# Optimization experiments

Measured on AMD Instinct MI355X. Metric: run time of the kernel, lower is better.

## Reference

```python
import jax, jax.numpy as jnp
import numpy as np

B, P, N = 64, 100, 1000
D, H, QD = 128, 8, 16
NUM_GROUPS = 5
MAX_DELTA = 4
SQRT_EMB = float(np.sqrt(D))
CLIP = 10.0
BIAS_INIT = 0.2
BIAS_TAU = 1.0


def setup_inputs() -> dict:
    key = jax.random.key(0)
    ks = jax.random.split(key, 12)
    w_scale = 1.0 / np.sqrt(D)
    encoded_nodes = jax.random.normal(ks[0], (B, N, D), dtype=jnp.float32)
    encoded_q1 = jax.random.normal(ks[1], (B, P, D), dtype=jnp.float32)
    encoded_last_node = jax.random.normal(ks[2], (B, P, D), dtype=jnp.float32)
    ninf_mask = jnp.where(jax.random.uniform(ks[3], (B, P, N)) < 0.2,
                          -jnp.inf, 0.0).astype(jnp.float32)
    Wq_first = (jax.random.normal(ks[4], (D, H * QD)) * w_scale).astype(jnp.float32)
    Wq_last = (jax.random.normal(ks[5], (D, H * QD)) * w_scale).astype(jnp.float32)
    Wk = (jax.random.normal(ks[6], (D, H * QD)) * w_scale).astype(jnp.float32)
    Wv = (jax.random.normal(ks[7], (D, H * QD)) * w_scale).astype(jnp.float32)
    W_comb = (jax.random.normal(ks[8], (H * QD, D)) * w_scale).astype(jnp.float32)
    b_comb = jnp.zeros((D,), dtype=jnp.float32)
    # learnable priority-bias table, init = 0.2 * exp(-delta / tau)
    deltas = jnp.arange(MAX_DELTA + 1, dtype=jnp.float32)
    bias_table = (BIAS_INIT * jnp.exp(-deltas / BIAS_TAU)).astype(jnp.float32)
    group_ids = jax.random.randint(ks[10], (B, N), 0, NUM_GROUPS).astype(jnp.int32)
    current_min_priority = jax.random.randint(ks[11], (B, P), 0, NUM_GROUPS).astype(jnp.int32)
    return {
        'encoded_nodes': encoded_nodes, 'encoded_q1': encoded_q1,
        'encoded_last_node': encoded_last_node, 'ninf_mask': ninf_mask,
        'Wq_first': Wq_first, 'Wq_last': Wq_last, 'Wk': Wk, 'Wv': Wv,
        'W_comb': W_comb, 'b_comb': b_comb, 'bias_table': bias_table,
        'group_ids': group_ids, 'current_min_priority': current_min_priority,
    }


def _heads(x):
    # [B, n, H*QD] -> [B, H, n, QD]
    b, n, _ = x.shape
    return x.reshape(b, n, H, QD).transpose(0, 2, 1, 3)


def reference(encoded_nodes, encoded_q1, encoded_last_node, ninf_mask,
              Wq_first, Wq_last, Wk, Wv, W_comb, b_comb, bias_table,
              group_ids, current_min_priority):
    # set_kv / set_q1
    k = _heads(encoded_nodes @ Wk)            # [B,H,N,QD]
    v = _heads(encoded_nodes @ Wv)            # [B,H,N,QD]
    q_first = _heads(encoded_q1 @ Wq_first)   # [B,H,P,QD]
    # forward
    q_last = _heads(encoded_last_node @ Wq_last)
    q = q_first + q_last
    score = jnp.einsum('bhpd,bhnd->bhpn', q, k) / jnp.sqrt(jnp.float32(QD))
    score = score + ninf_mask[:, None, :, :]  # rank3 ninf mask
    weights = jax.nn.softmax(score, axis=-1)
    out = jnp.einsum('bhpn,bhnd->bhpd', weights, v)
    out_concat = out.transpose(0, 2, 1, 3).reshape(B, P, H * QD)
    mh_atten_out = out_concat @ W_comb + b_comb  # [B,P,D]
    # single-head score against encoder embeddings
    score2 = jnp.einsum('bpd,bnd->bpn', mh_atten_out, encoded_nodes) / SQRT_EMB
    score_clipped = CLIP * jnp.tanh(score2)
    # relative-priority bias gather
    delta = jnp.clip(group_ids[:, None, :] - current_min_priority[:, :, None],
                     0, MAX_DELTA)                     # [B,P,N] int
    priority_bias = bias_table[delta]                  # gather
    priority_bias = jnp.where(jnp.isfinite(ninf_mask), priority_bias, 0.0)
    score_masked = score_clipped + priority_bias + ninf_mask
    probs = jax.nn.softmax(score_masked, axis=-1)
    return probs
```

## Files before the change

### kernel.cpp

```cpp
#include <hip/hip_runtime.h>

#define BB 64
#define PP 100
#define NN 1000
#define DDIM 128
#define HH 8
#define NSPL 8

typedef __attribute__((ext_vector_type(8))) short bf16x8;
typedef __attribute__((ext_vector_type(16))) float f32x16;
typedef __attribute__((ext_vector_type(4))) unsigned u32x4;
typedef __attribute__((ext_vector_type(2))) unsigned u32x2;

__device__ __forceinline__ unsigned bf16rne(float x) {
  unsigned u = __float_as_uint(x);
  return (u + 0x7FFFu + ((u >> 16) & 1u)) >> 16;
}
__device__ __forceinline__ unsigned pk_bf16(float a, float b) {
  return bf16rne(a) | (bf16rne(b) << 16);
}

__device__ __forceinline__ void split8(const float* __restrict__ p,
                                       bf16x8& hi8, bf16x8& lo8) {
  const float4 a = *(const float4*)p;
  const float4 c = *(const float4*)(p + 4);
  float v[8] = {a.x, a.y, a.z, a.w, c.x, c.y, c.z, c.w};
  unsigned hw[4], lw[4];
#pragma unroll
  for (int j = 0; j < 4; ++j) {
    const unsigned h0 = bf16rne(v[2*j]), h1 = bf16rne(v[2*j+1]);
    hw[j] = h0 | (h1 << 16);
    lw[j] = bf16rne(v[2*j]   - __uint_as_float(h0 << 16)) |
            (bf16rne(v[2*j+1] - __uint_as_float(h1 << 16)) << 16);
  }
  hi8 = __builtin_bit_cast(bf16x8, u32x4{hw[0], hw[1], hw[2], hw[3]});
  lo8 = __builtin_bit_cast(bf16x8, u32x4{lw[0], lw[1], lw[2], lw[3]});
}

__global__ __launch_bounds__(256) void pack_w_kernel(
    const float* __restrict__ W0, const float* __restrict__ W1,
    const float* __restrict__ W2, const float* __restrict__ W3,
    const float* __restrict__ W4, u32x4* __restrict__ wfrag)
{
  const int gid = blockIdx.x * 256 + threadIdx.x;
  const int mat = gid >> 11;
  const int ct = (gid >> 9) & 3;
  const int ks = (gid >> 6) & 7;
  const int lane = gid & 63;
  const float* __restrict__ W =
      (mat == 0) ? W0 : (mat == 1) ? W1 : (mat == 2) ? W2 : (mat == 3) ? W3 : W4;
  const int col = ct * 32 + (lane & 31);
  const int k0 = ks * 16 + (lane >> 5) * 8;
  unsigned hi[4], lo[4];
#pragma unroll
  for (int j = 0; j < 4; ++j) {
    const float x0 = W[(k0 + 2 * j) * DDIM + col];
    const float x1 = W[(k0 + 2 * j + 1) * DDIM + col];
    const unsigned h0 = bf16rne(x0), h1 = bf16rne(x1);
    hi[j] = h0 | (h1 << 16);
    lo[j] = bf16rne(x0 - __uint_as_float(h0 << 16)) |
            (bf16rne(x1 - __uint_as_float(h1 << 16)) << 16);
  }
  const int base = (((mat * 4 + ct) * 8 + ks) * 2) * 64 + lane;
  wfrag[base]      = u32x4{hi[0], hi[1], hi[2], hi[3]};
  wfrag[base + 64] = u32x4{lo[0], lo[1], lo[2], lo[3]};
}

__global__ __launch_bounds__(512) void pack_enc_kernel(
    const float* __restrict__ enc, u32x4* __restrict__ encp)
{
  const int b = blockIdx.x >> 5;
  const int t = blockIdx.x & 31;
  const int ks = threadIdx.x >> 6;
  const int lane = threadIdx.x & 63;
  const int n = min(32 * t + (lane & 31), NN - 1);
  const int k0 = ks * 16 + (lane >> 5) * 8;
  bf16x8 hi8, lo8;
  split8(enc + ((size_t)b * NN + n) * DDIM + k0, hi8, lo8);
  const size_t base = ((size_t)(b * 32 + t) * 8 + ks) * 128 + lane;
  encp[base]      = __builtin_bit_cast(u32x4, hi8);
  encp[base + 64] = __builtin_bit_cast(u32x4, lo8);
}

__global__ __launch_bounds__(512) void pack_mh_kernel(
    const float* __restrict__ mh, u32x4* __restrict__ mhp)
{
  const int b = blockIdx.x >> 2;
  const int mt = blockIdx.x & 3;
  const int ks = threadIdx.x >> 6;
  const int lane = threadIdx.x & 63;
  const int p = min(32 * mt + (lane & 31), PP - 1);
  const int k0 = ks * 16 + (lane >> 5) * 8;
  bf16x8 hi8, lo8;
  split8(mh + ((size_t)b * PP + p) * DDIM + k0, hi8, lo8);
  const size_t base = ((size_t)(b * 4 + mt) * 8 + ks) * 128 + lane;
  mhp[base]      = __builtin_bit_cast(u32x4, hi8);
  mhp[base + 64] = __builtin_bit_cast(u32x4, lo8);
}

__global__ __launch_bounds__(256) void proj_kv_mfma_kernel(
    const float* __restrict__ x, const u32x4* __restrict__ wfrag,
    float* __restrict__ outk, u32x4* __restrict__ vp)
{
  const int tid = threadIdx.x;
  const int lane = tid & 63;
  const int wid = tid >> 6;
  const int rtp = wid >> 1;
  const int ctp = wid & 1;
  const int b = blockIdx.x >> 3;
  const int blk8 = blockIdx.x & 7;
  const int rloc0 = blk8 * 128 + rtp * 64 + (lane & 31);
  const int kgrp = (lane >> 5) * 8;
  const int l31 = lane & 31;
  const float* xb = x + (size_t)b * NN * DDIM;

#pragma unroll 1
  for (int mat = 0; mat < 2; ++mat) {
    f32x16 acc[2][2];
#pragma unroll
    for (int a = 0; a < 2; ++a)
#pragma unroll
      for (int c = 0; c < 2; ++c)
#pragma unroll
        for (int i = 0; i < 16; ++i) acc[a][c][i] = 0.f;

#pragma unroll 1
    for (int ks = 0; ks < 8; ++ks) {
      bf16x8 ahi[2], alo[2];
#pragma unroll
      for (int rt = 0; rt < 2; ++rt) {
        const int arow = min(rloc0 + rt * 32, NN - 1);
        split8(xb + (size_t)arow * DDIM + ks * 16 + kgrp, ahi[rt], alo[rt]);
      }
#pragma unroll
      for (int ct = 0; ct < 2; ++ct) {
        const int c = ctp * 2 + ct;
        const int fo = (((mat * 4 + c) * 8 + ks) * 2) * 64 + lane;
        const bf16x8 bhi = __builtin_bit_cast(bf16x8, wfrag[fo]);
        const bf16x8 blo = __builtin_bit_cast(bf16x8, wfrag[fo + 64]);
#pragma unroll
        for (int rt = 0; rt < 2; ++rt) {
          acc[rt][ct] = __builtin_amdgcn_mfma_f32_32x32x16_bf16(
              ahi[rt], bhi, acc[rt][ct], 0, 0, 0);
          acc[rt][ct] = __builtin_amdgcn_mfma_f32_32x32x16_bf16(
              ahi[rt], blo, acc[rt][ct], 0, 0, 0);
          acc[rt][ct] = __builtin_amdgcn_mfma_f32_32x32x16_bf16(
              alo[rt], bhi, acc[rt][ct], 0, 0, 0);
        }
      }
    }

    if (mat == 0) {
#pragma unroll
      for (int rt = 0; rt < 2; ++rt)
#pragma unroll
        for (int ct = 0; ct < 2; ++ct) {
          const int colg = ctp * 64 + ct * 32 + l31;
          const int rowl0 = blk8 * 128 + rtp * 64 + rt * 32 + 4 * (lane >> 5);
#pragma unroll
          for (int r = 0; r < 16; ++r) {
            const int rowl = rowl0 + (r & 3) + 8 * (r >> 2);
            if (rowl < NN)
              outk[((size_t)b * NN + rowl) * DDIM + colg] = acc[rt][ct][r];
          }
        }
    } else {
#pragma unroll
      for (int rt = 0; rt < 2; ++rt) {
        const int t = blk8 * 4 + rtp * 2 + rt;
#pragma unroll
        for (int ct = 0; ct < 2; ++ct) {
          const int h = ctp * 4 + ct * 2 + (l31 >> 4);
          const int dcol = l31 & 15;
#pragma unroll
          for (int g = 0; g < 2; ++g) {
            unsigned hw[4], lw[4];
#pragma unroll
            for (int j = 0; j < 4; ++j) {
              const float a0 = acc[rt][ct][8 * g + 2 * j];
              const float a1 = acc[rt][ct][8 * g + 2 * j + 1];
              const unsigned h0 = bf16rne(a0), h1 = bf16rne(a1);
              hw[j] = h0 | (h1 << 16);
              lw[j] = bf16rne(a0 - __uint_as_float(h0 << 16)) |
                      (bf16rne(a1 - __uint_as_float(h1 << 16)) << 16);
            }
            const u32x2 rh0 = __builtin_amdgcn_permlane32_swap(hw[0], hw[2], false, false);
            const u32x2 rh1 = __builtin_amdgcn_permlane32_swap(hw[1], hw[3], false, false);
            const u32x2 rl0 = __builtin_amdgcn_permlane32_swap(lw[0], lw[2], false, false);
            const u32x2 rl1 = __builtin_amdgcn_permlane32_swap(lw[1], lw[3], false, false);
            const size_t sb = ((((size_t)(b * 32 + t) * 2 + g) * 8 + h) * 2) * 32
                              + (lane >> 5) * 16 + dcol;
            vp[sb]      = u32x4{rh0[0], rh1[0], rh0[1], rh1[1]};
            vp[sb + 32] = u32x4{rl0[0], rl1[0], rl0[1], rl1[1]};
          }
        }
      }
    }
  }
}

__global__ __launch_bounds__(256) void proj_q2_mfma_kernel(
    const float* __restrict__ x1, const float* __restrict__ x2,
    const u32x4* __restrict__ wfrag, float* __restrict__ out, float scale)
{
  const int tid = threadIdx.x;
  const int lane = tid & 63;
  const int w = tid >> 6;
  const int hi = lane >> 5;
  const int l31 = lane & 31;
  const int row0 = blockIdx.x * 128 + w * 32;
  const float* xr1 = x1 + (size_t)(row0 + l31) * DDIM + hi * 8;
  const float* xr2 = x2 + (size_t)(row0 + l31) * DDIM + hi * 8;

  f32x16 acc[4];
#pragma unroll
  for (int ct = 0; ct < 4; ++ct)
#pragma unroll
    for (int i = 0; i < 16; ++i) acc[ct][i] = 0.f;

#pragma unroll 1
  for (int ks = 0; ks < 8; ++ks) {
    bf16x8 a1h, a1l, a2h, a2l;
    split8(xr1 + ks * 16, a1h, a1l);
    split8(xr2 + ks * 16, a2h, a2l);
#pragma unroll
    for (int ct = 0; ct < 4; ++ct) {
      const int fo1 = (((2 * 4 + ct) * 8 + ks) * 2) * 64 + lane;
      const bf16x8 b1h = __builtin_bit_cast(bf16x8, wfrag[fo1]);
      const bf16x8 b1l = __builtin_bit_cast(bf16x8, wfrag[fo1 + 64]);
      acc[ct] = __builtin_amdgcn_mfma_f32_32x32x16_bf16(a1h, b1h, acc[ct], 0, 0, 0);
      acc[ct] = __builtin_amdgcn_mfma_f32_32x32x16_bf16(a1h, b1l, acc[ct], 0, 0, 0);
      acc[ct] = __builtin_amdgcn_mfma_f32_32x32x16_bf16(a1l, b1h, acc[ct], 0, 0, 0);
      const int fo2 = (((3 * 4 + ct) * 8 + ks) * 2) * 64 + lane;
      const bf16x8 b2h = __builtin_bit_cast(bf16x8, wfrag[fo2]);
      const bf16x8 b2l = __builtin_bit_cast(bf16x8, wfrag[fo2 + 64]);
      acc[ct] = __builtin_amdgcn_mfma_f32_32x32x16_bf16(a2h, b2h, acc[ct], 0, 0, 0);
      acc[ct] = __builtin_amdgcn_mfma_f32_32x32x16_bf16(a2h, b2l, acc[ct], 0, 0, 0);
      acc[ct] = __builtin_amdgcn_mfma_f32_32x32x16_bf16(a2l, b2h, acc[ct], 0, 0, 0);
    }
  }
#pragma unroll
  for (int ct = 0; ct < 4; ++ct) {
    const int colg = ct * 32 + l31;
    const int rowg0 = row0 + 4 * hi;
#pragma unroll
    for (int r = 0; r < 16; ++r) {
      const int rowg = rowg0 + (r & 3) + 8 * (r >> 2);
      out[(size_t)rowg * DDIM + colg] = acc[ct][r] * scale;
    }
  }
}

__global__ __launch_bounds__(256) void proj_comb_mfma_kernel(
    const float* __restrict__ x, const u32x4* __restrict__ wfrag,
    const float* __restrict__ bias, float* __restrict__ out)
{
  const int tid = threadIdx.x;
  const int lane = tid & 63;
  const int w = tid >> 6;
  const int hi = lane >> 5;
  const int l31 = lane & 31;
  const int row0 = blockIdx.x * 128 + w * 32;
  const float* xr = x + (size_t)(row0 + l31) * DDIM + hi * 8;

  f32x16 acc[4];
#pragma unroll
  for (int ct = 0; ct < 4; ++ct)
#pragma unroll
    for (int i = 0; i < 16; ++i) acc[ct][i] = 0.f;

#pragma unroll 1
  for (int ks = 0; ks < 8; ++ks) {
    bf16x8 ah, al;
    split8(xr + ks * 16, ah, al);
#pragma unroll
    for (int ct = 0; ct < 4; ++ct) {
      const int fo = (((4 * 4 + ct) * 8 + ks) * 2) * 64 + lane;
      const bf16x8 bh = __builtin_bit_cast(bf16x8, wfrag[fo]);
      const bf16x8 bl = __builtin_bit_cast(bf16x8, wfrag[fo + 64]);
      acc[ct] = __builtin_amdgcn_mfma_f32_32x32x16_bf16(ah, bh, acc[ct], 0, 0, 0);
      acc[ct] = __builtin_amdgcn_mfma_f32_32x32x16_bf16(ah, bl, acc[ct], 0, 0, 0);
      acc[ct] = __builtin_amdgcn_mfma_f32_32x32x16_bf16(al, bh, acc[ct], 0, 0, 0);
    }
  }
#pragma unroll
  for (int ct = 0; ct < 4; ++ct) {
    const int colg = ct * 32 + l31;
    const float bj = bias[colg];
    const int rowg0 = row0 + 4 * hi;
#pragma unroll
    for (int r = 0; r < 16; ++r) {
      const int rowg = rowg0 + (r & 3) + 8 * (r >> 2);
      out[(size_t)rowg * DDIM + colg] = acc[ct][r] + bj;
    }
  }
}

__global__ __launch_bounds__(512) void attn_mfma_kernel(
    const float* __restrict__ Q, const float* __restrict__ K,
    const u32x4* __restrict__ vp, const float* __restrict__ mask,
    float* __restrict__ po, float* __restrict__ lsum)
{
  __shared__ float mask_lds[PP * 132];

  const int b = blockIdx.x >> 3;
  const int chunk = blockIdx.x & 7;
  const int n0 = chunk * 128;
  const int tid = threadIdx.x;
  const int h = tid >> 6;
  const int l = tid & 63;
  const int hi = l >> 5;
  const int l31 = l & 31;

  const float NINF = -__builtin_huge_valf();
  for (int idx = tid; idx < PP * 32; idx += 512) {
    const int p = idx >> 5;
    const int c = idx & 31;
    const int nb4 = n0 + 4 * c;
    const int nsrc = min(nb4, NN - 4);
    float4 f = *(const float4*)(mask + ((size_t)(b * PP + p)) * NN + nsrc);
    f.x = (nb4 + 0 < NN) ? f.x : NINF;
    f.y = (nb4 + 1 < NN) ? f.y : NINF;
    f.z = (nb4 + 2 < NN) ? f.z : NINF;
    f.w = (nb4 + 3 < NN) ? f.w : NINF;
    *(float4*)&mask_lds[p * 132 + 4 * c] = f;
  }
  __syncthreads();

  bf16x8 qhi[4], qlo[4];
#pragma unroll
  for (int pt = 0; pt < 4; ++pt) {
    const int qrow = min(b * PP + pt * 32 + l31, BB * PP - 1);
    split8(Q + (size_t)qrow * DDIM + h * 16 + hi * 8, qhi[pt], qlo[pt]);
  }

  f32x16 oacc[4];
#pragma unroll
  for (int pt = 0; pt < 4; ++pt)
#pragma unroll
    for (int i = 0; i < 16; ++i) oacc[pt][i] = 0.f;
  float lacc[4] = {0.f, 0.f, 0.f, 0.f};

  const float* Kb = K + (size_t)b * NN * DDIM + h * 16;

#pragma unroll 1
  for (int nt = 0; nt < 4; ++nt) {
    const int nb = n0 + nt * 32;
    const int t = chunk * 4 + nt;

    bf16x8 khi, klo;
    {
      const int krow = min(nb + l31, NN - 1);
      split8(Kb + (size_t)krow * DDIM + hi * 8, khi, klo);
    }
    bf16x8 vhi[2], vlo[2];
#pragma unroll
    for (int ks = 0; ks < 2; ++ks) {
      const size_t sb = ((((size_t)(b * 32 + t) * 2 + ks) * 8 + h) * 2) * 32
                        + (size_t)hi * 16 + (l31 & 15);
      vhi[ks] = __builtin_bit_cast(bf16x8, vp[sb]);
      vlo[ks] = __builtin_bit_cast(bf16x8, vp[sb + 32]);
    }

#pragma unroll
    for (int pt = 0; pt < 4; ++pt) {
      const int prow = min(pt * 32 + l31, PP - 1);
      f32x16 s;
#pragma unroll
      for (int q = 0; q < 4; ++q) {
        const float4 f =
            *(const float4*)&mask_lds[prow * 132 + nt * 32 + q * 8 + hi * 4];
        s[4*q+0] = f.x; s[4*q+1] = f.y; s[4*q+2] = f.z; s[4*q+3] = f.w;
      }
      s = __builtin_amdgcn_mfma_f32_32x32x16_bf16(khi, qhi[pt], s, 0, 0, 0);
      s = __builtin_amdgcn_mfma_f32_32x32x16_bf16(khi, qlo[pt], s, 0, 0, 0);
      s = __builtin_amdgcn_mfma_f32_32x32x16_bf16(klo, qhi[pt], s, 0, 0, 0);

      float ev[16];
#pragma unroll
      for (int r = 0; r < 16; ++r) {
        const float e = __expf(s[r]);
        ev[r] = e;
        lacc[pt] += e;
      }
      unsigned u[8];
#pragma unroll
      for (int j = 0; j < 8; ++j) u[j] = pk_bf16(ev[2*j], ev[2*j+1]);
#pragma unroll
      for (int ks = 0; ks < 2; ++ks) {
        const unsigned t01 = u[ks*4+0], t23 = u[ks*4+1];
        const unsigned t45 = u[ks*4+2], t67 = u[ks*4+3];
        const u32x2 r0 = __builtin_amdgcn_permlane32_swap(t01, t45, false, false);
        const u32x2 r1 = __builtin_amdgcn_permlane32_swap(t23, t67, false, false);
        const bf16x8 pah = __builtin_bit_cast(bf16x8,
            u32x4{r0[0], r1[0], r0[1], r1[1]});
        oacc[pt] = __builtin_amdgcn_mfma_f32_32x32x16_bf16(pah, vhi[ks], oacc[pt], 0, 0, 0);
        oacc[pt] = __builtin_amdgcn_mfma_f32_32x32x16_bf16(pah, vlo[ks], oacc[pt], 0, 0, 0);
      }
    }
  }

  const int base = (b * NSPL + chunk) * PP;
#pragma unroll
  for (int pt = 0; pt < 4; ++pt) {
    const float ltot = lacc[pt] + __shfl_xor(lacc[pt], 32, 64);
    const int pl = pt * 32 + l31;
    if (l < 32 && pl < PP)
      lsum[(size_t)(base + pl) * HH + h] = ltot;
#pragma unroll
    for (int r = 0; r < 16; ++r) {
      const int p = pt * 32 + (r & 3) + 8 * (r >> 2) + 4 * hi;
      if (l31 < 16 && p < PP)
        po[(size_t)(base + p) * DDIM + h * 16 + l31] = oacc[pt][r];
    }
  }
}

__global__ __launch_bounds__(256) void merge_kernel(
    const float* __restrict__ po, const float* __restrict__ lsum,
    float* __restrict__ mh_in)
{
  const int idx = blockIdx.x * 256 + threadIdx.x;
  const int d = idx & 127;
  const int row = idx >> 7;
  const int b = row / PP;
  const int p = row - b * PP;
  const int h = d >> 4;
  float s = 0.f, lt = 0.f;
#pragma unroll
  for (int sp = 0; sp < NSPL; ++sp) {
    const int base = (b * NSPL + sp) * PP + p;
    s  += po[base * DDIM + d];
    lt += lsum[base * HH + h];
  }
  mh_in[idx] = s / lt;
}

__global__ __launch_bounds__(256) void score2_mfma_kernel(
    const u32x4* __restrict__ encp, const u32x4* __restrict__ mhp,
    const float* __restrict__ mask, const float* __restrict__ bias_table,
    const int* __restrict__ group_ids, const int* __restrict__ cur_min,
    float* __restrict__ out, float* __restrict__ ssum)
{
  const int b   = blockIdx.x >> 4;
  const int nc  = blockIdx.x & 15;
  const int n0  = nc * 64;
  const int tid = threadIdx.x;
  const int lane = tid & 63;
  const int mt   = tid >> 6;
  const int half = lane >> 5;
  const int l31  = lane & 31;

  f32x16 acc[2];
#pragma unroll
  for (int c = 0; c < 2; ++c)
#pragma unroll
    for (int i = 0; i < 16; ++i) acc[c][i] = 0.f;

  const u32x4* ma  = mhp  + ((size_t)(b * 4 + mt) * 8) * 128 + lane;
  const u32x4* eb0 = encp + ((size_t)(b * 32 + nc * 2) * 8) * 128 + lane;
  const u32x4* eb1 = encp + ((size_t)(b * 32 + nc * 2 + 1) * 8) * 128 + lane;

#pragma unroll 2
  for (int ks = 0; ks < 8; ++ks) {
    const bf16x8 ahi  = __builtin_bit_cast(bf16x8, ma[ks * 128]);
    const bf16x8 alo  = __builtin_bit_cast(bf16x8, ma[ks * 128 + 64]);
    const bf16x8 bhi0 = __builtin_bit_cast(bf16x8, eb0[ks * 128]);
    const bf16x8 blo0 = __builtin_bit_cast(bf16x8, eb0[ks * 128 + 64]);
    const bf16x8 bhi1 = __builtin_bit_cast(bf16x8, eb1[ks * 128]);
    const bf16x8 blo1 = __builtin_bit_cast(bf16x8, eb1[ks * 128 + 64]);
    acc[0] = __builtin_amdgcn_mfma_f32_32x32x16_bf16(ahi, bhi0, acc[0], 0, 0, 0);
    acc[0] = __builtin_amdgcn_mfma_f32_32x32x16_bf16(ahi, blo0, acc[0], 0, 0, 0);
    acc[0] = __builtin_amdgcn_mfma_f32_32x32x16_bf16(alo, bhi0, acc[0], 0, 0, 0);
    acc[1] = __builtin_amdgcn_mfma_f32_32x32x16_bf16(ahi, bhi1, acc[1], 0, 0, 0);
    acc[1] = __builtin_amdgcn_mfma_f32_32x32x16_bf16(ahi, blo1, acc[1], 0, 0, 0);
    acc[1] = __builtin_amdgcn_mfma_f32_32x32x16_bf16(alo, bhi1, acc[1], 0, 0, 0);
  }

  const float t0 = bias_table[0], t1 = bias_table[1], t2 = bias_table[2],
              t3 = bias_table[3], t4 = bias_table[4];
  const float two_inv_sqrt_emb = 0.1767766952966369f;

  int cmpv[16];
#pragma unroll
  for (int r = 0; r < 16; ++r) {
    const int p = 32 * mt + (r & 3) + 8 * (r >> 2) + 4 * half;
    cmpv[r] = cur_min[b * PP + min(p, PP - 1)];
  }

  float rsum[16];
#pragma unroll
  for (int r = 0; r < 16; ++r) rsum[r] = 0.f;

#pragma unroll
  for (int ct = 0; ct < 2; ++ct) {
    const int n = n0 + ct * 32 + l31;
    const bool nvalid = n < NN;
    const int nr = nvalid ? n : NN - 1;
    const int gid = group_ids[b * NN + nr];
#pragma unroll
    for (int r = 0; r < 16; ++r) {
      const int p = 32 * mt + (r & 3) + 8 * (r >> 2) + 4 * half;
      const bool pvalid = p < PP;
      const int pr = pvalid ? p : PP - 1;
      const float m = mask[((size_t)(b * PP + pr)) * NN + nr];
      const float ex = __expf(acc[ct][r] * two_inv_sqrt_emb);
      const float sc = 10.0f - 20.0f / (ex + 1.0f);
      int delta = gid - cmpv[r];
      delta = delta < 0 ? 0 : (delta > 4 ? 4 : delta);
      const float pb = (delta == 0) ? t0 : (delta == 1) ? t1 : (delta == 2) ? t2
                     : (delta == 3) ? t3 : t4;
      float e = (nvalid && pvalid) ? __expf(sc + pb + m) : 0.0f;
      if (nvalid && pvalid) out[((size_t)(b * PP + p)) * NN + n] = e;
      rsum[r] += e;
    }
  }
#pragma unroll
  for (int r = 0; r < 16; ++r) {
    float ws = rsum[r];
#pragma unroll
    for (int off = 1; off < 32; off <<= 1) ws += __shfl_xor(ws, off, 64);
    rsum[r] = ws;
  }
  if (l31 == 0) {
#pragma unroll
    for (int r = 0; r < 16; ++r) {
      const int p = 32 * mt + (r & 3) + 8 * (r >> 2) + 4 * half;
      if (p < PP) ssum[(size_t)(b * PP + p) * 16 + nc] = rsum[r];
    }
  }
}

__global__ __launch_bounds__(256) void norm_kernel(
    const float* __restrict__ ssum, float* __restrict__ out)
{
  const int row = blockIdx.x;
  float s = 0.f;
#pragma unroll
  for (int i = 0; i < 16; ++i) s += ssum[(size_t)row * 16 + i];
  const float inv = 1.0f / s;
#pragma unroll
  for (int i = 0; i < 4; ++i) {
    const int c = i * 256 + (int)threadIdx.x;
    if (c < NN) out[(size_t)row * NN + c] *= inv;
  }
}

extern "C" void kernel_launch(void* const* d_in, const int* in_sizes, int n_in,
                              void* d_out, int out_size, void* d_ws, size_t ws_size,
                              hipStream_t stream)
{
  (void)in_sizes; (void)n_in; (void)out_size; (void)ws_size;
  const float* enc_nodes  = (const float*)d_in[0];
  const float* enc_q1     = (const float*)d_in[1];
  const float* enc_last   = (const float*)d_in[2];
  const float* ninf       = (const float*)d_in[3];
  const float* Wq_first   = (const float*)d_in[4];
  const float* Wq_last    = (const float*)d_in[5];
  const float* Wk         = (const float*)d_in[6];
  const float* Wv         = (const float*)d_in[7];
  const float* W_comb     = (const float*)d_in[8];
  const float* b_comb     = (const float*)d_in[9];
  const float* bias_table = (const float*)d_in[10];
  const int*   group_ids  = (const int*)d_in[11];
  const int*   cur_min    = (const int*)d_in[12];
  float* out = (float*)d_out;
  float* ws  = (float*)d_ws;

  float* Qw = ws;
  float* Kw = Qw + 819200;
  u32x4* Vp = (u32x4*)(Kw + 8192000);
  float* po = Kw + 8192000 + 8388608;
  float* ls = po + 6553600;
  float* mh = ls + 409600;
  float* sm = mh + 819200;

  u32x4* wfrag = (u32x4*)sm;
  u32x4* encp = (u32x4*)Kw;
  u32x4* mhp  = ((u32x4*)Kw) + 2097152;

  pack_w_kernel<<<40, 256, 0, stream>>>(Wk, Wv, Wq_first, Wq_last, W_comb, wfrag);
  proj_q2_mfma_kernel<<<BB*PP/128, 256, 0, stream>>>(enc_q1, enc_last, wfrag,
                                                     Qw, 0.25f);
  proj_kv_mfma_kernel<<<BB*8, 256, 0, stream>>>(enc_nodes, wfrag, Kw, Vp);
  attn_mfma_kernel<<<BB*NSPL, 512, 0, stream>>>(Qw, Kw, Vp, ninf, po, ls);
  merge_kernel<<<3200, 256, 0, stream>>>(po, ls, Qw);
  pack_enc_kernel<<<BB*32, 512, 0, stream>>>(enc_nodes, encp);
  proj_comb_mfma_kernel<<<BB*PP/128, 256, 0, stream>>>(Qw, wfrag, b_comb, mh);
  pack_mh_kernel<<<BB*4, 512, 0, stream>>>(mh, mhp);
  score2_mfma_kernel<<<BB*16, 256, 0, stream>>>(encp, mhp, ninf, bias_table,
                                                group_ids, cur_min, out, sm);
  norm_kernel<<<BB*PP, 256, 0, stream>>>(sm, out);
}
```

Measured before the change: 177.8 us.

## Pre-pack K as bf16 hi/lo fragments and replace float mask with bitmask

The K projection now writes K directly as split bf16 hi/lo MFMA fragments, transposed through per-wave LDS, instead of fp32 rows that the attention kernel re-split. A new kernel compresses the -inf mask into 32-bit bitmasks, so attention no longer stages a full float mask tile in LDS. Masking is applied by zeroing exp values. The attention grid is split by head halves into 256-thread blocks for more blocks and less LDS. This adds an extra launch and assumes the mask holds only 0 or -inf, consistent with the task's input definition.

Result: slower. 188.0 us (median of 3 runs) (+5.7%).

```diff
diff --git a/kernel.cpp b/kernel.cpp
--- a/kernel.cpp
+++ b/kernel.cpp
@@ -64,6 +64,36 @@
   const int base = (((mat * 4 + ct) * 8 + ks) * 2) * 64 + lane;
   wfrag[base]      = u32x4{hi[0], hi[1], hi[2], hi[3]};
   wfrag[base + 64] = u32x4{lo[0], lo[1], lo[2], lo[3]};
+}
+
+__global__ __launch_bounds__(256) void pack_bits_kernel(
+    const float* __restrict__ mask, unsigned* __restrict__ bits)
+{
+  const int gid = blockIdx.x * 256 + threadIdx.x;
+  const int w = gid & 31;
+  const int row = gid >> 5;
+  const float* mrow = mask + (size_t)row * NN + w * 32;
+  const float NINF = -__builtin_huge_valf();
+  unsigned u = 0;
+  if (w < 31) {
+#pragma unroll
+    for (int k = 0; k < 8; ++k) {
+      const float4 m = *(const float4*)(mrow + 4 * k);
+      u |= (m.x == NINF ? 1u : 0u) << (4 * k);
+      u |= (m.y == NINF ? 1u : 0u) << (4 * k + 1);
+      u |= (m.z == NINF ? 1u : 0u) << (4 * k + 2);
+      u |= (m.w == NINF ? 1u : 0u) << (4 * k + 3);
+    }
+  } else {
+#pragma unroll
+    for (int j = 0; j < 32; ++j) {
+      const int n = 992 + j;
+      unsigned bit = 1u;
+      if (n < NN) bit = (mrow[j] == NINF) ? 1u : 0u;
+      u |= bit << j;
+    }
+  }
+  bits[gid] = u;
 }
 
 __global__ __launch_bounds__(512) void pack_enc_kernel(
@@ -100,8 +130,9 @@
 
 __global__ __launch_bounds__(256) void proj_kv_mfma_kernel(
     const float* __restrict__ x, const u32x4* __restrict__ wfrag,
-    float* __restrict__ outk, u32x4* __restrict__ vp)
-{
+    u32x4* __restrict__ kp, u32x4* __restrict__ vp)
+{
+  __shared__ float tile[4][32 * 33];
   const int tid = threadIdx.x;
   const int lane = tid & 63;
   const int wid = tid >> 6;
@@ -113,6 +144,7 @@
   const int kgrp = (lane >> 5) * 8;
   const int l31 = lane & 31;
   const float* xb = x + (size_t)b * NN * DDIM;
+  float* mytile = tile[wid];
 
 #pragma unroll 1
   for (int mat = 0; mat < 2; ++mat) {
@@ -155,13 +187,30 @@
       for (int rt = 0; rt < 2; ++rt)
 #pragma unroll
         for (int ct = 0; ct < 2; ++ct) {
-          const int colg = ctp * 64 + ct * 32 + l31;
-          const int rowl0 = blk8 * 128 + rtp * 64 + rt * 32 + 4 * (lane >> 5);
-#pragma unroll
-          for (int r = 0; r < 16; ++r) {
-            const int rowl = rowl0 + (r & 3) + 8 * (r >> 2);
-            if (rowl < NN)
-              outk[((size_t)b * NN + rowl) * DDIM + colg] = acc[rt][ct][r];
+#pragma unroll
+          for (int r = 0; r < 16; ++r)
+            mytile[((r & 3) + 8 * (r >> 2) + 4 * (lane >> 5)) * 33 + l31] =
+                acc[rt][ct][r];
+          asm volatile("s_waitcnt lgkmcnt(0)" ::: "memory");
+          const int t = blk8 * 4 + rtp * 2 + rt;
+#pragma unroll
+          for (int hl = 0; hl < 2; ++hl) {
+            const int h = ctp * 4 + ct * 2 + hl;
+            float v[8];
+#pragma unroll
+            for (int i = 0; i < 8; ++i)
+              v[i] = mytile[l31 * 33 + hl * 16 + kgrp + i];
+            unsigned hw[4], lw[4];
+#pragma unroll
+            for (int j = 0; j < 4; ++j) {
+              const unsigned h0 = bf16rne(v[2*j]), h1 = bf16rne(v[2*j+1]);
+              hw[j] = h0 | (h1 << 16);
+              lw[j] = bf16rne(v[2*j]   - __uint_as_float(h0 << 16)) |
+                      (bf16rne(v[2*j+1] - __uint_as_float(h1 << 16)) << 16);
+            }
+            const size_t kb = (((size_t)(b * 32 + t) * 8 + h) * 2) * 64 + lane;
+            kp[kb]      = u32x4{hw[0], hw[1], hw[2], hw[3]};
+            kp[kb + 64] = u32x4{lw[0], lw[1], lw[2], lw[3]};
           }
         }
     } else {
@@ -296,37 +345,20 @@
   }
 }
 
-__global__ __launch_bounds__(512) void attn_mfma_kernel(
-    const float* __restrict__ Q, const float* __restrict__ K,
-    const u32x4* __restrict__ vp, const float* __restrict__ mask,
+__global__ __launch_bounds__(256) void attn_mfma_kernel(
+    const float* __restrict__ Q, const u32x4* __restrict__ kp,
+    const u32x4* __restrict__ vp, const unsigned* __restrict__ bits,
     float* __restrict__ po, float* __restrict__ lsum)
 {
-  __shared__ float mask_lds[PP * 132];
-
-  const int b = blockIdx.x >> 3;
-  const int chunk = blockIdx.x & 7;
-  const int n0 = chunk * 128;
+  const int b = blockIdx.x >> 4;
+  const int chunk = (blockIdx.x >> 1) & 7;
+  const int hh = blockIdx.x & 1;
   const int tid = threadIdx.x;
-  const int h = tid >> 6;
+  const int h = hh * 4 + (tid >> 6);
   const int l = tid & 63;
   const int hi = l >> 5;
   const int l31 = l & 31;
 
-  const float NINF = -__builtin_huge_valf();
-  for (int idx = tid; idx < PP * 32; idx += 512) {
-    const int p = idx >> 5;
-    const int c = idx & 31;
-    const int nb4 = n0 + 4 * c;
-    const int nsrc = min(nb4, NN - 4);
-    float4 f = *(const float4*)(mask + ((size_t)(b * PP + p)) * NN + nsrc);
-    f.x = (nb4 + 0 < NN) ? f.x : NINF;
-    f.y = (nb4 + 1 < NN) ? f.y : NINF;
-    f.z = (nb4 + 2 < NN) ? f.z : NINF;
-    f.w = (nb4 + 3 < NN) ? f.w : NINF;
-    *(float4*)&mask_lds[p * 132 + 4 * c] = f;
-  }
-  __syncthreads();
-
   bf16x8 qhi[4], qlo[4];
 #pragma unroll
   for (int pt = 0; pt < 4; ++pt) {
@@ -341,18 +373,13 @@
     for (int i = 0; i < 16; ++i) oacc[pt][i] = 0.f;
   float lacc[4] = {0.f, 0.f, 0.f, 0.f};
 
-  const float* Kb = K + (size_t)b * NN * DDIM + h * 16;
-
 #pragma unroll 1
   for (int nt = 0; nt < 4; ++nt) {
-    const int nb = n0 + nt * 32;
     const int t = chunk * 4 + nt;
 
-    bf16x8 khi, klo;
-    {
-      const int krow = min(nb + l31, NN - 1);
-      split8(Kb + (size_t)krow * DDIM + hi * 8, khi, klo);
-    }
+    const size_t kb = (((size_t)(b * 32 + t) * 8 + h) * 2) * 64 + l;
+    const bf16x8 khi = __builtin_bit_cast(bf16x8, kp[kb]);
+    const bf16x8 klo = __builtin_bit_cast(bf16x8, kp[kb + 64]);
     bf16x8 vhi[2], vlo[2];
 #pragma unroll
     for (int ks = 0; ks < 2; ++ks) {
@@ -361,17 +388,18 @@
       vhi[ks] = __builtin_bit_cast(bf16x8, vp[sb]);
       vlo[ks] = __builtin_bit_cast(bf16x8, vp[sb + 32]);
     }
-
+    unsigned wbits[4];
 #pragma unroll
     for (int pt = 0; pt < 4; ++pt) {
       const int prow = min(pt * 32 + l31, PP - 1);
+      wbits[pt] = bits[(size_t)(b * PP + prow) * 32 + chunk * 4 + nt];
+    }
+
+#pragma unroll
+    for (int pt = 0; pt < 4; ++pt) {
       f32x16 s;
 #pragma unroll
-      for (int q = 0; q < 4; ++q) {
-        const float4 f =
-            *(const float4*)&mask_lds[prow * 132 + nt * 32 + q * 8 + hi * 4];
-        s[4*q+0] = f.x; s[4*q+1] = f.y; s[4*q+2] = f.z; s[4*q+3] = f.w;
-      }
+      for (int i = 0; i < 16; ++i) s[i] = 0.f;
       s = __builtin_amdgcn_mfma_f32_32x32x16_bf16(khi, qhi[pt], s, 0, 0, 0);
       s = __builtin_amdgcn_mfma_f32_32x32x16_bf16(khi, qlo[pt], s, 0, 0, 0);
       s = __builtin_amdgcn_mfma_f32_32x32x16_bf16(klo, qhi[pt], s, 0, 0, 0);
@@ -379,9 +407,11 @@
       float ev[16];
 #pragma unroll
       for (int r = 0; r < 16; ++r) {
+        const int j = (r & 3) + 8 * (r >> 2) + 4 * hi;
+        const bool masked = (wbits[pt] >> j) & 1;
         const float e = __expf(s[r]);
-        ev[r] = e;
-        lacc[pt] += e;
+        ev[r] = masked ? 0.f : e;
+        lacc[pt] += ev[r];
       }
       unsigned u[8];
 #pragma unroll
@@ -568,22 +598,24 @@
   float* ws  = (float*)d_ws;
 
   float* Qw = ws;
-  float* Kw = Qw + 819200;
-  u32x4* Vp = (u32x4*)(Kw + 8192000);
-  float* po = Kw + 8192000 + 8388608;
+  u32x4* Kp = (u32x4*)(Qw + 819200);
+  u32x4* Vp = Kp + 2097152;
+  float* po = (float*)(Vp + 2097152);
   float* ls = po + 6553600;
   float* mh = ls + 409600;
   float* sm = mh + 819200;
 
   u32x4* wfrag = (u32x4*)sm;
-  u32x4* encp = (u32x4*)Kw;
-  u32x4* mhp  = ((u32x4*)Kw) + 2097152;
+  unsigned* bits = (unsigned*)mh;
+  u32x4* encp = Kp;
+  u32x4* mhp  = Kp + 2097152;
 
   pack_w_kernel<<<40, 256, 0, stream>>>(Wk, Wv, Wq_first, Wq_last, W_comb, wfrag);
+  pack_bits_kernel<<<800, 256, 0, stream>>>(ninf, bits);
   proj_q2_mfma_kernel<<<BB*PP/128, 256, 0, stream>>>(enc_q1, enc_last, wfrag,
                                                      Qw, 0.25f);
-  proj_kv_mfma_kernel<<<BB*8, 256, 0, stream>>>(enc_nodes, wfrag, Kw, Vp);
-  attn_mfma_kernel<<<BB*NSPL, 512, 0, stream>>>(Qw, Kw, Vp, ninf, po, ls);
+  proj_kv_mfma_kernel<<<BB*8, 256, 0, stream>>>(enc_nodes, wfrag, Kp, Vp);
+  attn_mfma_kernel<<<BB*NSPL*2, 256, 0, stream>>>(Qw, Kp, Vp, bits, po, ls);
   merge_kernel<<<3200, 256, 0, stream>>>(po, ls, Qw);
   pack_enc_kernel<<<BB*32, 512, 0, stream>>>(enc_nodes, encp);
   proj_comb_mfma_kernel<<<BB*PP/128, 256, 0, stream>>>(Qw, wfrag, b_comb, mh);
```
